# Performance work log

Hardware: AMD Instinct MI355X
Metric: run time of the kernel (lower is better)

The kernel has to match this reference:

```python
import jax, jax.numpy as jnp
import numpy as np

Z_DIM = 3
H = 128
N_BLOCKS = 4
N = 30000
E = 180000
T = 2


def _mlp2(x, W1, b1, W2, b2):
    return jnp.maximum(x @ W1 + b1, 0.0) @ W2 + b2


def _stats(x, eps=1e-8):
    # batch mean/std as accumulated by the running-stat Normalizer (buffers -> no grad)
    m = x.mean(0)
    v = jnp.maximum((x * x).mean(0) - m * m, 0.0)
    s = jnp.maximum(jnp.sqrt(v), eps)
    return jax.lax.stop_gradient(m), jax.lax.stop_gradient(s)


def setup_inputs() -> dict:
    key = jax.random.key(0)
    ks = jax.random.split(key, 32)

    def w(k, shape, fan_in):
        return jax.random.normal(k, shape, jnp.float32) / np.sqrt(fan_in).astype(np.float32)

    inp = {}
    inp["z"] = jax.random.normal(ks[0], (T, N, Z_DIM), jnp.float32)
    inp["z_target"] = jax.random.normal(ks[1], (N, Z_DIM), jnp.float32)
    inp["pos"] = jax.random.uniform(ks[2], (N, 2), jnp.float32)
    # encoder node MLP: z_dim -> H -> H
    inp["enc_node_W1"] = w(ks[3], (Z_DIM, H), Z_DIM)
    inp["enc_node_b1"] = jnp.zeros((H,), jnp.float32)
    inp["enc_node_W2"] = w(ks[4], (H, H), H)
    inp["enc_node_b2"] = jnp.zeros((H,), jnp.float32)
    # encoder edge MLP: edge_dim(3) -> H -> H
    inp["enc_edge_W1"] = w(ks[5], (3, H), 3)
    inp["enc_edge_b1"] = jnp.zeros((H,), jnp.float32)
    inp["enc_edge_W2"] = w(ks[6], (H, H), H)
    inp["enc_edge_b2"] = jnp.zeros((H,), jnp.float32)
    # decoder MLP: H -> H -> z_dim
    inp["dec_W1"] = w(ks[7], (H, H), H)
    inp["dec_b1"] = jnp.zeros((H,), jnp.float32)
    inp["dec_W2"] = w(ks[8], (H, Z_DIM), H)
    inp["dec_b2"] = jnp.zeros((Z_DIM,), jnp.float32)
    # GraphNetBlocks, stacked over n_blocks
    inp["blk_edge_W1"] = w(ks[9], (N_BLOCKS, 3 * H, H), 3 * H)
    inp["blk_edge_b1"] = jnp.zeros((N_BLOCKS, H), jnp.float32)
    inp["blk_edge_W2"] = w(ks[10], (N_BLOCKS, H, H), H)
    inp["blk_edge_b2"] = jnp.zeros((N_BLOCKS, H), jnp.float32)
    inp["blk_node_W1"] = w(ks[11], (N_BLOCKS, 2 * H, H), 2 * H)
    inp["blk_node_b1"] = jnp.zeros((N_BLOCKS, H), jnp.float32)
    inp["blk_node_W2"] = w(ks[12], (N_BLOCKS, H, H), H)
    inp["blk_node_b2"] = jnp.zeros((N_BLOCKS, H), jnp.float32)
    # bidirectional mesh edges (triangles_to_edges output)
    inp["senders"] = jax.random.randint(ks[13], (E,), 0, N, jnp.int64)
    inp["receivers"] = jax.random.randint(ks[14], (E,), 0, N, jnp.int64)
    return inp


def reference(z, z_target, pos,
              enc_node_W1, enc_node_b1, enc_node_W2, enc_node_b2,
              enc_edge_W1, enc_edge_b1, enc_edge_W2, enc_edge_b2,
              dec_W1, dec_b1, dec_W2, dec_b2,
              blk_edge_W1, blk_edge_b1, blk_edge_W2, blk_edge_b2,
              blk_node_W1, blk_node_b1, blk_node_W2, blk_node_b2,
              senders, receivers):
    zl = z[-1]                                   # [N, z_dim]
    n_nodes = zl.shape[0]

    # --- build_graph ---
    rel = pos[senders] - pos[receivers]          # [E, 2]
    ef_raw = jnp.concatenate([rel, jnp.linalg.norm(rel, axis=1, keepdims=True)], axis=1)  # [E, 3]
    em, es = _stats(ef_raw)
    ef = _mlp2((ef_raw - em) / es, enc_edge_W1, enc_edge_b1, enc_edge_W2, enc_edge_b2)    # [E, H]
    nm, ns = _stats(zl)
    nf = _mlp2((zl - nm) / ns, enc_node_W1, enc_node_b1, enc_node_W2, enc_node_b2)        # [N, H]

    # --- message passing blocks ---
    def block(carry, p):
        nf, ef = carry
        eW1, eb1, eW2, eb2, nW1, nb1, nW2, nb2 = p
        e_in = jnp.concatenate([ef, nf[senders], nf[receivers]], axis=1)   # [E, 3H]
        ef = _mlp2(e_in, eW1, eb1, eW2, eb2) + ef
        agg = jax.ops.segment_sum(ef, receivers, num_segments=n_nodes)    # [N, H]
        n_in = jnp.concatenate([nf, agg], axis=1)                          # [N, 2H]
        nf = _mlp2(n_in, nW1, nb1, nW2, nb2) + nf
        return (nf, ef), None

    (nf, ef), _ = jax.lax.scan(block, (nf, ef),
                               (blk_edge_W1, blk_edge_b1, blk_edge_W2, blk_edge_b2,
                                blk_node_W1, blk_node_b1, blk_node_W2, blk_node_b2))

    # --- decode + loss ---
    output = _mlp2(nf, dec_W1, dec_b1, dec_W2, dec_b2)                     # [N, z_dim]
    target = z_target - zl
    om, os = _stats(target)
    target_normalized = (target - om) / os
    loss = jnp.mean((target_normalized - output) ** 2)

    z_update = jax.lax.stop_gradient(output) * os + om                     # Normalizer.inverse(detach)
    z_pred = zl + z_update
    rmse = jnp.mean(jnp.sqrt(jnp.mean((z_pred - z_target) ** 2, axis=0)))
    return z_pred, loss, rmse
```

## Files before the change

### kernel.cpp

```cpp
#include <hip/hip_runtime.h>
#include <hip/hip_bf16.h>
#include <math.h>

#define HDIM 128
#define TPB 256

typedef __attribute__((ext_vector_type(8))) short bf16x8;
typedef __attribute__((ext_vector_type(4))) float f32x4;

static inline int ceil_div(int a, int b){ return (a + b - 1) / b; }

__device__ __forceinline__ float wave_sum(float v){
#pragma unroll
  for (int o = 32; o > 0; o >>= 1) v += __shfl_down(v, o, 64);
  return v;
}
__device__ __forceinline__ int wave_sum_i(int v){
#pragma unroll
  for (int o = 32; o > 0; o >>= 1) v += __shfl_down(v, o, 64);
  return v;
}

__device__ __forceinline__ short f2bf(float f){
  __hip_bfloat16 h = __float2bfloat16(f);
  return *reinterpret_cast<short*>(&h);
}
__device__ __forceinline__ float bfb2f(short s){
  unsigned int u = ((unsigned int)(unsigned short)s) << 16;
  return __builtin_bit_cast(float, u);
}

__device__ __forceinline__ void gl_lds16(const short* g, short* l){
  __builtin_amdgcn_global_load_lds(
      (const __attribute__((address_space(1))) void*)g,
      (__attribute__((address_space(3))) void*)l, 16, 0, 0);
}

__global__ void prep_a(const int* __restrict__ rcv, int* __restrict__ deg, int E, int neb,
                       const float* __restrict__ zl, const float* __restrict__ zt,
                       float* __restrict__ npart, int N, int nnb,
                       const float* __restrict__ encEW2,
                       const float* __restrict__ encNW2,
                       const float* __restrict__ decW1,
                       const float* __restrict__ beW1,
                       const float* __restrict__ beW2,
                       const float* __restrict__ bnW1,
                       const float* __restrict__ bnW2,
                       __hip_bfloat16* __restrict__ wp){
  __shared__ float red[4][12];
  const int bx = blockIdx.x, tid = threadIdx.x;
  if (bx < neb){
    int e = bx * 256 + tid;
    if (e < E) atomicAdd(&deg[rcv[e]], 1);
    return;
  }
  if (bx < neb + nnb){
    int b = bx - neb;
    int w = tid >> 6, l = tid & 63;
    int n = b * 256 + tid;
    float s[12];
#pragma unroll
    for (int i = 0; i < 12; i++) s[i] = 0.f;
    if (n < N){
#pragma unroll
      for (int d = 0; d < 3; d++){
        float z = zl[3*n+d];
        float t = zt[3*n+d] - z;
        s[d]   = z;  s[3+d] = z*z;
        s[6+d] = t;  s[9+d] = t*t;
      }
    }
#pragma unroll
    for (int i = 0; i < 12; i++) s[i] = wave_sum(s[i]);
    if (l == 0)
#pragma unroll
      for (int i = 0; i < 12; i++) red[w][i] = s[i];
    __syncthreads();
    if (tid < 12)
      npart[(size_t)b * 12 + tid] =
        red[0][tid] + red[1][tid] + red[2][tid] + red[3][tid];
    return;
  }
  int pid = bx - neb - nnb;
  int y = pid / 192;
  int x = pid - y * 192;
  const float* src; __hip_bfloat16* dst; int K;
  if (y == 0){ src = encEW2; dst = wp;          K = 128; }
  else if (y == 1){ src = encNW2; dst = wp + 16384; K = 128; }
  else if (y == 2){ src = decW1;  dst = wp + 32768; K = 128; }
  else {
    int b = (y - 3) >> 2, j = (y - 3) & 3;
    __hip_bfloat16* base = wp + 49152 + b * 114688;
    if (j == 0){ src = beW1 + b*49152; dst = base;          K = 384; }
    else if (j == 1){ src = beW2 + b*16384; dst = base + 49152; K = 128; }
    else if (j == 2){ src = bnW1 + b*32768; dst = base + 65536; K = 256; }
    else { src = bnW2 + b*16384; dst = base + 98304; K = 128; }
  }
  int id = x * 256 + tid;
  if (id >= 128 * K) return;
  int c = id >> 12;
  int r = id & 4095;
  int t = r >> 9;
  int l = (r >> 3) & 63;
  int j = r & 7;
  int k = c * 32 + ((l >> 4) << 3) + j;
  int n = t * 16 + (l & 15);
  dst[id] = __float2bfloat16(src[k * 128 + n]);
}

__global__ void scan_pass1(const int* __restrict__ deg, int* __restrict__ bsum, int N){
  __shared__ int red[4];
  int tid = threadIdx.x;
  int base = blockIdx.x * 1024;
  int s = 0;
  for (int i = tid; i < 1024; i += 256){
    int idx = base + i;
    if (idx < N) s += deg[idx];
  }
  s = wave_sum_i(s);
  if ((tid & 63) == 0) red[tid >> 6] = s;
  __syncthreads();
  if (tid == 0) bsum[blockIdx.x] = red[0] + red[1] + red[2] + red[3];
}

__global__ void scan_pass3(const int* __restrict__ deg, const int* __restrict__ bsum,
                           int nsb, int* __restrict__ cursor, int N){
  __shared__ int tsum[256];
  __shared__ int base_s;
  int tid = threadIdx.x;
  if (tid == 0){
    int acc = 0;
    for (int b = 0; b < (int)blockIdx.x; b++) acc += bsum[b];
    base_s = acc;
  }
  int base = blockIdx.x * 1024;
  int i0 = base + tid * 4;
  int v[4];
  int s = 0;
#pragma unroll
  for (int k = 0; k < 4; k++){
    int idx = i0 + k;
    v[k] = (idx < N) ? deg[idx] : 0;
    s += v[k];
  }
  tsum[tid] = s;
  __syncthreads();
  for (int off = 1; off < 256; off <<= 1){
    int val = (tid >= off) ? tsum[tid - off] : 0;
    __syncthreads();
    tsum[tid] += val;
    __syncthreads();
  }
  int excl = (tid == 0) ? 0 : tsum[tid - 1];
  int b = base_s + excl;
#pragma unroll
  for (int k = 0; k < 4; k++){
    int idx = i0 + k;
    if (idx < N){
      cursor[idx] = b;
      b += v[k];
    }
  }
}

__global__ void edge_prep(const float* __restrict__ pos,
                          const int* __restrict__ snd,
                          const int* __restrict__ rcv,
                          int* __restrict__ cursor,
                          int* __restrict__ psnd,
                          int* __restrict__ prcv,
                          float* __restrict__ ef_raw,
                          float* __restrict__ epart,
                          const float* __restrict__ npart, int nn,
                          float* __restrict__ fin,
                          unsigned int* __restrict__ ep_cnt,
                          int E, int N){
  __shared__ float red[4][6];
  __shared__ float rawS[18];
  __shared__ float redS[4];
  __shared__ int doneS;
  int tid = threadIdx.x, w = tid >> 6, l = tid & 63;
  int e = blockIdx.x * blockDim.x + tid;
  float s[6] = {0.f,0.f,0.f,0.f,0.f,0.f};
  if (e < E){
    int si = snd[e], ri = rcv[e];
    int p = atomicAdd(&cursor[ri], 1);
    psnd[p] = si;
    prcv[p] = ri;
    float rx = pos[2*si]   - pos[2*ri];
    float ry = pos[2*si+1] - pos[2*ri+1];
    float nm = sqrtf(rx*rx + ry*ry);
    ef_raw[3*p]   = rx;
    ef_raw[3*p+1] = ry;
    ef_raw[3*p+2] = nm;
    s[0] = rx; s[1] = ry; s[2] = nm;
    s[3] = rx*rx; s[4] = ry*ry; s[5] = nm*nm;
  }
#pragma unroll
  for (int k = 0; k < 6; k++) s[k] = wave_sum(s[k]);
  if (l == 0)
#pragma unroll
    for (int k = 0; k < 6; k++) red[w][k] = s[k];
  __syncthreads();
  if (tid < 6)
    epart[(size_t)blockIdx.x * 6 + tid] =
      red[0][tid] + red[1][tid] + red[2][tid] + red[3][tid];
  __syncthreads();
  if (tid == 0){
    __threadfence();
    unsigned int t = atomicAdd(ep_cnt, 1u);
    doneS = (t == gridDim.x - 1);
  }
  __syncthreads();
  if (!doneS) return;
  const int ne = gridDim.x;
  for (int j = 0; j < 6; j++){
    float t = 0.f;
    for (int b = tid; b < ne; b += 256) t += epart[(size_t)b * 6 + j];
    t = wave_sum(t);
    if (l == 0) redS[w] = t;
    __syncthreads();
    if (tid == 0) rawS[j] = redS[0] + redS[1] + redS[2] + redS[3];
    __syncthreads();
  }
  for (int j = 0; j < 12; j++){
    float t = 0.f;
    for (int b = tid; b < nn; b += 256) t += npart[(size_t)b * 12 + j];
    t = wave_sum(t);
    if (l == 0) redS[w] = t;
    __syncthreads();
    if (tid == 0) rawS[6 + j] = redS[0] + redS[1] + redS[2] + redS[3];
    __syncthreads();
  }
  if (tid == 0){
#pragma unroll
    for (int d = 0; d < 3; d++){
      float cE = (float)E, cN = (float)N;
      float m, v;
      m = rawS[0+d] / cE; v = fmaxf(rawS[3+d]/cE - m*m, 0.f);
      fin[0+d] = m;  fin[3+d]  = fmaxf(sqrtf(v), 1e-8f);
      m = rawS[6+d] / cN; v = fmaxf(rawS[9+d]/cN - m*m, 0.f);
      fin[6+d] = m;  fin[9+d]  = fmaxf(sqrtf(v), 1e-8f);
      m = rawS[12+d] / cN; v = fmaxf(rawS[15+d]/cN - m*m, 0.f);
      fin[12+d] = m; fin[15+d] = fmaxf(sqrtf(v), 1e-8f);
    }
  }
}

__launch_bounds__(256)
__global__ void encoder_both(const float* __restrict__ eraw,
                             const float* __restrict__ zl,
                             const float* __restrict__ fin,
                             const float* __restrict__ eW1, const float* __restrict__ eb1,
                             const float* __restrict__ nW1, const float* __restrict__ nb1,
                             const __hip_bfloat16* __restrict__ wp,
                             const float* __restrict__ eb2, const float* __restrict__ nb2,
                             __hip_bfloat16* __restrict__ efo, __hip_bfloat16* __restrict__ nfo,
                             int E, int N, int EB){
  __shared__ __align__(16) short bsh[16384];
  const int tid = threadIdx.x, w = tid >> 6, l = tid & 63, m = l & 15, q = l >> 4;
  const bool ise = ((int)blockIdx.x < EB);
  const float* raw = ise ? eraw : zl;
  const float* mptr = fin + (ise ? 0 : 6);
  const float* sptr = fin + (ise ? 3 : 9);
  const float* W1 = ise ? eW1 : nW1;
  const float* b1 = ise ? eb1 : nb1;
  const float* b2 = ise ? eb2 : nb2;
  const short* wsrc = (const short*)wp + (ise ? 0 : 16384);
  __hip_bfloat16* out = ise ? efo : nfo;
  const int rows = ise ? E : N;
  const int bx = ise ? (int)blockIdx.x : (int)blockIdx.x - EB;
#pragma unroll
  for (int i = 0; i < 8; i++){
    int inst = w * 8 + i;
    gl_lds16(wsrc + inst * 512 + l * 8, &bsh[inst * 512]);
  }
  float s0 = mptr[0], s1 = mptr[1], s2 = mptr[2];
  float d0 = sptr[0], d1 = sptr[1], d2 = sptr[2];
  const int row0 = bx * 64 + w * 16;
  const int ra = min(row0 + m, rows - 1);
  float x0 = (raw[3*ra]   - s0) / d0;
  float x1 = (raw[3*ra+1] - s1) / d1;
  float x2 = (raw[3*ra+2] - s2) / d2;
  bf16x8 afr[4];
#pragma unroll
  for (int c = 0; c < 4; c++){
    int nb = c * 32 + q * 8;
#pragma unroll
    for (int j = 0; j < 8; j++){
      float h = b1[nb+j] + x0 * W1[nb+j] + x1 * W1[128+nb+j] + x2 * W1[256+nb+j];
      afr[c][j] = f2bf(fmaxf(h, 0.f));
    }
  }
  f32x4 acc[8];
#pragma unroll
  for (int t = 0; t < 8; t++) acc[t] = (f32x4){0.f,0.f,0.f,0.f};
  __syncthreads();
#pragma unroll
  for (int c = 0; c < 4; c++){
#pragma unroll
    for (int t = 0; t < 8; t++){
      bf16x8 b = *(const bf16x8*)&bsh[(c*8 + t)*512 + l*8];
      acc[t] = __builtin_amdgcn_mfma_f32_16x16x32_bf16(afr[c], b, acc[t], 0, 0, 0);
    }
  }
  const int row_d = row0 + q * 4;
#pragma unroll
  for (int t = 0; t < 8; t++){
    int col = t * 16 + m;
    float bb = b2[col];
#pragma unroll
    for (int r = 0; r < 4; r++){
      int e = row_d + r;
      if (e < rows) out[(size_t)e * HDIM + col] = __float2bfloat16(acc[t][r] + bb);
    }
  }
}

__launch_bounds__(256)
__global__ void msg_pre(const __hip_bfloat16* __restrict__ nf,
                        const __hip_bfloat16* __restrict__ eWf,
                        __hip_bfloat16* __restrict__ u,
                        float* __restrict__ agg, int N){
  __shared__ __align__(16) short wsh[16384];
  const int tid = threadIdx.x, w = tid >> 6, l = tid & 63, m = l & 15, q = l >> 4;
  const short* wsrc = (const short*)eWf + 4 * 4096;
#pragma unroll
  for (int i = 0; i < 8; i++){
    int f = w * 8 + i;
    gl_lds16(wsrc + f * 512 + l * 8, &wsh[f * 512]);
  }
  {
    float* az = agg + (size_t)blockIdx.x * 8192;
#pragma unroll
    for (int i = 0; i < 8; i++)
      *(f32x4*)(az + (size_t)(i * 256 + tid) * 4) = (f32x4){0.f,0.f,0.f,0.f};
  }
  const int row0 = blockIdx.x * 64 + w * 16;
  const int ra = min(row0 + m, N - 1);
  const short* pa = (const short*)nf + (size_t)ra * HDIM + q * 8;
  bf16x8 afr[4];
#pragma unroll
  for (int c = 0; c < 4; c++) afr[c] = *(const bf16x8*)(pa + c * 32);
  f32x4 acc[8];
#pragma unroll
  for (int t = 0; t < 8; t++) acc[t] = (f32x4){0.f,0.f,0.f,0.f};
  __syncthreads();
#pragma unroll
  for (int c = 0; c < 4; c++)
#pragma unroll
    for (int t = 0; t < 8; t++){
      bf16x8 b = *(const bf16x8*)&wsh[(c*8 + t)*512 + l*8];
      acc[t] = __builtin_amdgcn_mfma_f32_16x16x32_bf16(afr[c], b, acc[t], 0, 0, 0);
    }
  const int row_d = row0 + q * 4;
#pragma unroll
  for (int t = 0; t < 8; t++){
    int col = t * 16 + m;
#pragma unroll
    for (int r = 0; r < 4; r++){
      int n = row_d + r;
      if (n < N) u[(size_t)n * 256 + col] = __float2bfloat16(acc[t][r]);
    }
  }
  __syncthreads();
#pragma unroll
  for (int i = 0; i < 8; i++){
    int f = w * 8 + i;
    gl_lds16(wsrc + 16384 + f * 512 + l * 8, &wsh[f * 512]);
  }
#pragma unroll
  for (int t = 0; t < 8; t++) acc[t] = (f32x4){0.f,0.f,0.f,0.f};
  __syncthreads();
#pragma unroll
  for (int c = 0; c < 4; c++)
#pragma unroll
    for (int t = 0; t < 8; t++){
      bf16x8 b = *(const bf16x8*)&wsh[(c*8 + t)*512 + l*8];
      acc[t] = __builtin_amdgcn_mfma_f32_16x16x32_bf16(afr[c], b, acc[t], 0, 0, 0);
    }
#pragma unroll
  for (int t = 0; t < 8; t++){
    int col = 128 + t * 16 + m;
#pragma unroll
    for (int r = 0; r < 4; r++){
      int n = row_d + r;
      if (n < N) u[(size_t)n * 256 + col] = __float2bfloat16(acc[t][r]);
    }
  }
}

__launch_bounds__(512)
__global__ void edge_block(const int* __restrict__ psnd,
                           const int* __restrict__ prcv,
                           const __hip_bfloat16* __restrict__ u,
                           __hip_bfloat16* __restrict__ ef,
                           const __hip_bfloat16* __restrict__ Wfrag,
                           const float* __restrict__ b1,
                           const float* __restrict__ b2,
                           float* __restrict__ agg,
                           int do_write, int E){
  __shared__ __align__(16) short bsh[16384];
  __shared__ __align__(16) short hsh[8][16][136];
  __shared__ int rsh[128];
  const int tid = threadIdx.x, w = tid >> 6, l = tid & 63, m = l & 15, q = l >> 4;
  const short* wsrc = (const short*)Wfrag;
  const int row0 = blockIdx.x * 128 + w * 16;
  const int grow = min(row0 + (l >> 2), E - 1);
  const int us_row = psnd[grow], ur_row = prcv[grow];
  if ((l & 3) == 0) rsh[w * 16 + (l >> 2)] = ur_row;
#pragma unroll
  for (int i = 0; i < 4; i++){
    int inst = i * 8 + w;
    gl_lds16(wsrc + inst * 512 + l * 8, &bsh[inst * 512]);
  }
  const int ra = min(row0 + m, E - 1);
  const short* pe = (const short*)ef + (size_t)ra * HDIM + q * 8;
  bf16x8 afr[4];
#pragma unroll
  for (int c = 0; c < 4; c++) afr[c] = *(const bf16x8*)(pe + c * 32);
  {
    const short* pus = (const short*)u + (size_t)us_row * 256 + (l & 3) * 32;
    const short* pur = (const short*)u + (size_t)ur_row * 256 + 128 + (l & 3) * 32;
    short* hdst = &hsh[w][l >> 2][(l & 3) * 32];
#pragma unroll
    for (int k = 0; k < 4; k++){
      bf16x8 a = *(const bf16x8*)(pus + k * 8);
      bf16x8 b = *(const bf16x8*)(pur + k * 8);
      bf16x8 s;
#pragma unroll
      for (int j = 0; j < 8; j++) s[j] = f2bf(bfb2f(a[j]) + bfb2f(b[j]));
      *(bf16x8*)(hdst + k * 8) = s;
    }
  }
  f32x4 acc[8];
#pragma unroll
  for (int t = 0; t < 8; t++) acc[t] = (f32x4){0.f,0.f,0.f,0.f};
  __syncthreads();
#pragma unroll
  for (int c = 0; c < 4; c++){
#pragma unroll
    for (int t = 0; t < 8; t++){
      bf16x8 b = *(const bf16x8*)&bsh[(c*8 + t)*512 + l*8];
      acc[t] = __builtin_amdgcn_mfma_f32_16x16x32_bf16(afr[c], b, acc[t], 0, 0, 0);
    }
  }
  __syncthreads();
#pragma unroll
  for (int i = 0; i < 4; i++){
    int inst = i * 8 + w;
    gl_lds16(wsrc + 49152 + inst * 512 + l * 8, &bsh[inst * 512]);
  }
#pragma unroll
  for (int t = 0; t < 8; t++){
    float bb = b1[t * 16 + m];
#pragma unroll
    for (int r = 0; r < 4; r++){
      float uval = bfb2f(hsh[w][q*4 + r][t*16 + m]);
      hsh[w][q*4 + r][t*16 + m] = f2bf(fmaxf(acc[t][r] + uval + bb, 0.f));
    }
  }
  __syncthreads();
  bf16x8 ah[4];
  const short* ph = &hsh[w][m][0] + q * 8;
#pragma unroll
  for (int c = 0; c < 4; c++) ah[c] = *(const bf16x8*)(ph + c * 32);
#pragma unroll
  for (int t = 0; t < 8; t++) acc[t] = (f32x4){0.f,0.f,0.f,0.f};
#pragma unroll
  for (int c = 0; c < 4; c++){
#pragma unroll
    for (int t = 0; t < 8; t++){
      bf16x8 b = *(const bf16x8*)&bsh[(c*8 + t)*512 + l*8];
      acc[t] = __builtin_amdgcn_mfma_f32_16x16x32_bf16(ah[c], b, acc[t], 0, 0, 0);
    }
  }
#pragma unroll
  for (int t = 0; t < 8; t++){
    float bb = b2[t * 16 + m];
#pragma unroll
    for (int r = 0; r < 4; r++)
      hsh[w][q*4 + r][t*16 + m] = f2bf(acc[t][r] + bb);
  }
  const int orow = row0 + (l >> 2);
  const int orc = min(orow, E - 1);
  const short* pold = (const short*)ef + (size_t)orc * HDIM + (l & 3) * 32;
  short* hslot = &hsh[w][l >> 2][(l & 3) * 32];
  short* dst = (short*)ef + (size_t)orc * HDIM + (l & 3) * 32;
  const bool wr = (orow < E) && do_write;
#pragma unroll
  for (int k = 0; k < 4; k++){
    bf16x8 vnew = *(const bf16x8*)(hslot + k * 8);
    bf16x8 vo   = *(const bf16x8*)(pold + k * 8);
    bf16x8 vr;
#pragma unroll
    for (int j = 0; j < 8; j++) vr[j] = f2bf(bfb2f(vnew[j]) + bfb2f(vo[j]));
    *(bf16x8*)(hslot + k * 8) = vr;
    if (wr) *(bf16x8*)(dst + k * 8) = vr;
  }
  __syncthreads();
  {
    const int c = tid & 127;
    const int g = tid >> 7;
    const int nval = min(128, E - (int)blockIdx.x * 128);
    const int e0 = g * 32;
    if (e0 < nval){
      const int e1 = min(e0 + 32, nval);
      float run = 0.f; int cur = -1; int runstart = e0;
#pragma unroll
      for (int half = 0; half < 2; half++){
        float v[16]; int rv[16];
#pragma unroll
        for (int k = 0; k < 16; k++){
          int e = e0 + half * 16 + k;
          v[k]  = bfb2f(hsh[(e >> 4) & 7][e & 15][c]);
          rv[k] = rsh[e & 127];
        }
#pragma unroll
        for (int k = 0; k < 16; k++){
          int e = e0 + half * 16 + k;
          if (e < e1){
            if (rv[k] != cur){
              if (cur >= 0){
                if (runstart == e0) atomicAdd(&agg[(size_t)cur * 128 + c], run);
                else                agg[(size_t)cur * 128 + c] = run;
              }
              cur = rv[k]; run = 0.f; runstart = e;
            }
            run += v[k];
          }
        }
      }
      atomicAdd(&agg[(size_t)cur * 128 + c], run);
    }
  }
}

#define NB_COMPUTE_CHUNK(c) do {                                               \
  const short* bb_ = &bsh[(((c) >> 1) & 1) * 8192 + ((c) & 1) * 4096];         \
  _Pragma("unroll")                                                            \
  for (int t = 0; t < 8; t++){                                                 \
    bf16x8 b = *(const bf16x8*)(bb_ + t * 512 + l * 8);                        \
    acc[t] = __builtin_amdgcn_mfma_f32_16x16x32_bf16(afr[c], b, acc[t], 0, 0, 0); \
  }                                                                            \
} while(0)

__launch_bounds__(256)
__global__ void node_block(const float* __restrict__ agg,
                           __hip_bfloat16* __restrict__ nf,
                           const __hip_bfloat16* __restrict__ Wfrag,
                           const float* __restrict__ b1,
                           const float* __restrict__ b2,
                           const __hip_bfloat16* __restrict__ eWf_next,
                           __hip_bfloat16* __restrict__ u,
                           float* __restrict__ aggz,
                           int mode,
                           const __hip_bfloat16* __restrict__ decWf,
                           const float* __restrict__ db1,
                           const float* __restrict__ dW2,
                           const float* __restrict__ db2,
                           const float* __restrict__ zl,
                           const float* __restrict__ z_target,
                           const float* __restrict__ fin,
                           float* __restrict__ d_out,
                           float* __restrict__ lred,
                           unsigned int* __restrict__ cnt,
                           int N){
  __shared__ __align__(16) short bsh[16384];
  __shared__ __align__(16) short hsh[4][16][136];
  __shared__ float Wl[HDIM * 3];
  __shared__ float redS[4][4];
  const int tid = threadIdx.x, w = tid >> 6, l = tid & 63, m = l & 15, q = l >> 4;
  const short* wsrc = (const short*)Wfrag;
  auto stage_pair = [&](int p){
    const short* s = wsrc + p * 8192;
    short* d = &bsh[(p & 1) * 8192];
#pragma unroll
    for (int i = 0; i < 4; i++)
      gl_lds16(s + (i*4 + w)*512 + l*8, d + (i*4 + w)*512);
  };
  stage_pair(0); stage_pair(1);

  const int row0 = blockIdx.x * 64 + w * 16;
  const int ra = min(row0 + m, N - 1);
  const short* pn = (const short*)nf + (size_t)ra * HDIM + q * 8;
  bf16x8 afr[8];
#pragma unroll
  for (int c = 0; c < 4; c++) afr[c] = *(const bf16x8*)(pn + c * 32);

  const float* pag = agg + (size_t)ra * 128 + q * 8;
#pragma unroll
  for (int c = 0; c < 4; c++){
    f32x4 a0 = *(const f32x4*)(pag + c * 32);
    f32x4 a1 = *(const f32x4*)(pag + c * 32 + 4);
#pragma unroll
    for (int j = 0; j < 4; j++){
      afr[4 + c][j]     = f2bf(a0[j]);
      afr[4 + c][4 + j] = f2bf(a1[j]);
    }
  }

  f32x4 acc[8];
#pragma unroll
  for (int t = 0; t < 8; t++) acc[t] = (f32x4){0.f,0.f,0.f,0.f};
  __syncthreads();
  if (mode == 0){
    float* az = aggz + (size_t)blockIdx.x * 8192;
#pragma unroll
    for (int i = 0; i < 8; i++)
      *(f32x4*)(az + (size_t)(i * 256 + tid) * 4) = (f32x4){0.f,0.f,0.f,0.f};
  }
  NB_COMPUTE_CHUNK(0);
  NB_COMPUTE_CHUNK(1);
  __syncthreads();
  stage_pair(2);
  NB_COMPUTE_CHUNK(2);
  NB_COMPUTE_CHUNK(3);
  __syncthreads();
  stage_pair(3);
  NB_COMPUTE_CHUNK(4);
  NB_COMPUTE_CHUNK(5);
  __syncthreads();
  NB_COMPUTE_CHUNK(6);
  NB_COMPUTE_CHUNK(7);
  __syncthreads();
  {
    const short* s = wsrc + 32768;
#pragma unroll
    for (int i = 0; i < 8; i++)
      gl_lds16(s + (i*4 + w)*512 + l*8, &bsh[(i*4 + w)*512]);
  }
#pragma unroll
  for (int t = 0; t < 8; t++){
    float bb = b1[t * 16 + m];
#pragma unroll
    for (int r = 0; r < 4; r++)
      hsh[w][q*4 + r][t*16 + m] = f2bf(fmaxf(acc[t][r] + bb, 0.f));
  }
  __syncthreads();
  const short* ph = &hsh[w][m][0] + q * 8;
#pragma unroll
  for (int t = 0; t < 8; t++) acc[t] = (f32x4){0.f,0.f,0.f,0.f};
#pragma unroll
  for (int c = 0; c < 4; c++){
    bf16x8 a = *(const bf16x8*)(ph + c * 32);
#pragma unroll
    for (int t = 0; t < 8; t++){
      bf16x8 b = *(const bf16x8*)&bsh[(c*8 + t)*512 + l*8];
      acc[t] = __builtin_amdgcn_mfma_f32_16x16x32_bf16(a, b, acc[t], 0, 0, 0);
    }
  }
#pragma unroll
  for (int t = 0; t < 8; t++){
    float bb = b2[t * 16 + m];
#pragma unroll
    for (int r = 0; r < 4; r++)
      hsh[w][q*4 + r][t*16 + m] = f2bf(acc[t][r] + bb);
  }
  {
    const int orow = row0 + (l >> 2);
    const int orc = min(orow, N - 1);
    const short* pold = (const short*)nf + (size_t)orc * HDIM + (l & 3) * 32;
    short* hslot = &hsh[w][l >> 2][(l & 3) * 32];
    short* dst = (short*)nf + (size_t)orc * HDIM + (l & 3) * 32;
    const bool wr = (orow < N) && (mode == 0);
#pragma unroll
    for (int k = 0; k < 4; k++){
      bf16x8 vnew = *(const bf16x8*)(hslot + k * 8);
      bf16x8 vo   = *(const bf16x8*)(pold + k * 8);
      bf16x8 vr;
#pragma unroll
      for (int j = 0; j < 8; j++) vr[j] = f2bf(bfb2f(vnew[j]) + bfb2f(vo[j]));
      *(bf16x8*)(hslot + k * 8) = vr;
      if (wr) *(bf16x8*)(dst + k * 8) = vr;
    }
  }

  if (mode == 0){
    const short* ws = (const short*)eWf_next + 4 * 4096;
#pragma unroll
    for (int i = 0; i < 8; i++){
      int f = w * 8 + i;
      gl_lds16(ws + f * 512 + l * 8, &bsh[f * 512]);
    }
    __syncthreads();
    bf16x8 a2[4];
    const short* ph2 = &hsh[w][m][0] + q * 8;
#pragma unroll
    for (int c = 0; c < 4; c++) a2[c] = *(const bf16x8*)(ph2 + c * 32);
#pragma unroll
    for (int t = 0; t < 8; t++) acc[t] = (f32x4){0.f,0.f,0.f,0.f};
#pragma unroll
    for (int c = 0; c < 4; c++)
#pragma unroll
      for (int t = 0; t < 8; t++){
        bf16x8 b = *(const bf16x8*)&bsh[(c*8 + t)*512 + l*8];
        acc[t] = __builtin_amdgcn_mfma_f32_16x16x32_bf16(a2[c], b, acc[t], 0, 0, 0);
      }
    const int row_d = row0 + q * 4;
#pragma unroll
    for (int t = 0; t < 8; t++){
      int col = t * 16 + m;
#pragma unroll
      for (int r = 0; r < 4; r++){
        int n = row_d + r;
        if (n < N) u[(size_t)n * 256 + col] = __float2bfloat16(acc[t][r]);
      }
    }
    __syncthreads();
#pragma unroll
    for (int i = 0; i < 8; i++){
      int f = w * 8 + i;
      gl_lds16(ws + 16384 + f * 512 + l * 8, &bsh[f * 512]);
    }
#pragma unroll
    for (int t = 0; t < 8; t++) acc[t] = (f32x4){0.f,0.f,0.f,0.f};
    __syncthreads();
#pragma unroll
    for (int c = 0; c < 4; c++)
#pragma unroll
      for (int t = 0; t < 8; t++){
        bf16x8 b = *(const bf16x8*)&bsh[(c*8 + t)*512 + l*8];
        acc[t] = __builtin_amdgcn_mfma_f32_16x16x32_bf16(a2[c], b, acc[t], 0, 0, 0);
      }
#pragma unroll
    for (int t = 0; t < 8; t++){
      int col = 128 + t * 16 + m;
#pragma unroll
      for (int r = 0; r < 4; r++){
        int n = row_d + r;
        if (n < N) u[(size_t)n * 256 + col] = __float2bfloat16(acc[t][r]);
      }
    }
  } else {
    const short* ws = (const short*)decWf;
#pragma unroll
    for (int i = 0; i < 8; i++){
      int f = w * 8 + i;
      gl_lds16(ws + f * 512 + l * 8, &bsh[f * 512]);
    }
    for (int i = tid; i < HDIM * 3; i += 256) Wl[i] = dW2[i];
    __syncthreads();
    bf16x8 a2[4];
    const short* ph2 = &hsh[w][m][0] + q * 8;
#pragma unroll
    for (int c = 0; c < 4; c++) a2[c] = *(const bf16x8*)(ph2 + c * 32);
#pragma unroll
    for (int t = 0; t < 8; t++) acc[t] = (f32x4){0.f,0.f,0.f,0.f};
#pragma unroll
    for (int c = 0; c < 4; c++)
#pragma unroll
      for (int t = 0; t < 8; t++){
        bf16x8 b = *(const bf16x8*)&bsh[(c*8 + t)*512 + l*8];
        acc[t] = __builtin_amdgcn_mfma_f32_16x16x32_bf16(a2[c], b, acc[t], 0, 0, 0);
      }
    float p0[4] = {0,0,0,0}, p1[4] = {0,0,0,0}, p2[4] = {0,0,0,0};
#pragma unroll
    for (int t = 0; t < 8; t++){
      int col = t * 16 + m;
      float bb = db1[col];
      float w0 = Wl[col*3], w1 = Wl[col*3+1], w2 = Wl[col*3+2];
#pragma unroll
      for (int r = 0; r < 4; r++){
        float h = fmaxf(acc[t][r] + bb, 0.f);
        p0[r] += h * w0; p1[r] += h * w1; p2[r] += h * w2;
      }
    }
#pragma unroll
    for (int r = 0; r < 4; r++){
#pragma unroll
      for (int o = 1; o < 16; o <<= 1){
        p0[r] += __shfl_xor(p0[r], o, 64);
        p1[r] += __shfl_xor(p1[r], o, 64);
        p2[r] += __shfl_xor(p2[r], o, 64);
      }
    }
    float s[4] = {0.f,0.f,0.f,0.f};
    if (m == 0){
#pragma unroll
      for (int r = 0; r < 4; r++){
        int n = row0 + q * 4 + r;
        if (n < N){
          float pd[3] = {p0[r], p1[r], p2[r]};
#pragma unroll
          for (int d = 0; d < 3; d++){
            float o   = pd[d] + db2[d];
            float om = fin[12 + d], os = fin[15 + d];
            float zld = zl[3*n + d];
            float zt  = z_target[3*n + d];
            float tn  = ((zt - zld) - om) / os;
            float diff = tn - o;
            s[0] += diff * diff;
            float zp = zld + o * os + om;
            d_out[3*n + d] = zp;
            float e = zp - zt;
            s[1 + d] += e * e;
          }
        }
      }
    }
#pragma unroll
    for (int k = 0; k < 4; k++) s[k] = wave_sum(s[k]);
    if (l == 0)
#pragma unroll
      for (int k = 0; k < 4; k++) redS[w][k] = s[k];
    __syncthreads();
    if (tid < 4)
      atomicAdd(&lred[tid], redS[0][tid] + redS[1][tid] + redS[2][tid] + redS[3][tid]);
    __syncthreads();
    if (tid == 0){
      __threadfence();
      unsigned int t = atomicAdd(cnt, 1u);
      if (t == gridDim.x - 1){
        float vals[4];
#pragma unroll
        for (int k = 0; k < 4; k++) vals[k] = atomicAdd(&lred[k], 0.f);
        float cN = (float)N;
        float loss = vals[0] / (3.f * cN);
        float rmse = (sqrtf(vals[1]/cN) + sqrtf(vals[2]/cN) + sqrtf(vals[3]/cN)) / 3.f;
        d_out[(size_t)3 * N]     = loss;
        d_out[(size_t)3 * N + 1] = rmse;
      }
    }
  }
}

extern "C" void kernel_launch(void* const* d_in, const int* in_sizes, int n_in,
                              void* d_out, int out_size, void* d_ws, size_t ws_size,
                              hipStream_t stream){
  const float* z           = (const float*)d_in[0];
  const float* z_target    = (const float*)d_in[1];
  const float* pos         = (const float*)d_in[2];
  const float* enc_node_W1 = (const float*)d_in[3];
  const float* enc_node_b1 = (const float*)d_in[4];
  const float* enc_node_W2 = (const float*)d_in[5];
  const float* enc_node_b2 = (const float*)d_in[6];
  const float* enc_edge_W1 = (const float*)d_in[7];
  const float* enc_edge_b1 = (const float*)d_in[8];
  const float* enc_edge_W2 = (const float*)d_in[9];
  const float* enc_edge_b2 = (const float*)d_in[10];
  const float* dec_W1      = (const float*)d_in[11];
  const float* dec_b1      = (const float*)d_in[12];
  const float* dec_W2      = (const float*)d_in[13];
  const float* dec_b2      = (const float*)d_in[14];
  const float* blk_edge_W1 = (const float*)d_in[15];
  const float* blk_edge_b1 = (const float*)d_in[16];
  const float* blk_edge_W2 = (const float*)d_in[17];
  const float* blk_edge_b2 = (const float*)d_in[18];
  const float* blk_node_W1 = (const float*)d_in[19];
  const float* blk_node_b1 = (const float*)d_in[20];
  const float* blk_node_W2 = (const float*)d_in[21];
  const float* blk_node_b2 = (const float*)d_in[22];
  const int*   senders     = (const int*)d_in[23];
  const int*   receivers   = (const int*)d_in[24];

  const int N = in_sizes[1] / 3;
  const int E = in_sizes[23];
  const float* zl = z + (size_t)N * 3;

  const int neb = ceil_div(E, TPB);
  const int nnb = ceil_div(N, TPB);
  const int nsb = ceil_div(N, 1024);
  const int EB  = ceil_div(E, 64);
  const int NB  = ceil_div(N, 64);

  char* p = (char*)d_ws;
  auto carve = [&](size_t bytes) -> char* {
    char* r = p; p += (bytes + 255) & ~(size_t)255; return r;
  };
  float* stats_fin = (float*)carve(32 * 4);
  float* epart     = (float*)carve((size_t)neb * 6 * 4);
  float* npart     = (float*)carve((size_t)nnb * 12 * 4);
  float* ef_raw    = (float*)carve((size_t)E * 3 * 4);
  int*   deg       = (int*)carve((size_t)(N + 16) * 4);
  float* lred      = (float*)(deg + N);
  unsigned int* cnt    = (unsigned int*)(deg + N + 4);
  unsigned int* ep_cnt = (unsigned int*)(deg + N + 5);
  int*   bsum      = (int*)carve((size_t)(nsb + 1) * 4);
  int*   cursor    = (int*)carve((size_t)N * 4);
  int*   psnd      = (int*)carve((size_t)E * 4);
  int*   prcv      = (int*)carve((size_t)E * 4);
  float* agg       = (float*)carve(((size_t)N + 64) * 128 * 4);
  __hip_bfloat16* wp = (__hip_bfloat16*)carve((size_t)507904 * 2);
  __hip_bfloat16* ef = (__hip_bfloat16*)carve((size_t)E * HDIM * 2);
  __hip_bfloat16* nf = (__hip_bfloat16*)carve((size_t)N * HDIM * 2);
  __hip_bfloat16* u  = (__hip_bfloat16*)carve((size_t)N * 256 * 2);

  float* out = (float*)d_out;

  hipMemsetAsync(deg, 0, (size_t)(N + 16) * 4, stream);

  prep_a<<<neb + nnb + 3648, TPB, 0, stream>>>(receivers, deg, E, neb,
                                               zl, z_target, npart, N, nnb,
                                               enc_edge_W2, enc_node_W2, dec_W1,
                                               blk_edge_W1, blk_edge_W2,
                                               blk_node_W1, blk_node_W2, wp);
  scan_pass1<<<nsb, TPB, 0, stream>>>(deg, bsum, N);
  scan_pass3<<<nsb, TPB, 0, stream>>>(deg, bsum, nsb, cursor, N);
  edge_prep<<<neb, TPB, 0, stream>>>(pos, senders, receivers, cursor,
                                     psnd, prcv, ef_raw, epart,
                                     npart, nnb, stats_fin, ep_cnt, E, N);

  encoder_both<<<EB + NB, TPB, 0, stream>>>(ef_raw, zl, stats_fin,
                                            enc_edge_W1, enc_edge_b1,
                                            enc_node_W1, enc_node_b1,
                                            wp, enc_edge_b2, enc_node_b2,
                                            ef, nf, E, N, EB);

  msg_pre<<<NB, TPB, 0, stream>>>(nf, wp + 49152, u, agg, N);

  for (int b = 0; b < 4; b++){
    const __hip_bfloat16* eWf = wp + 49152 + (size_t)b * 114688;
    const __hip_bfloat16* nWf = eWf + 65536;
    const float* eb1 = blk_edge_b1 + (size_t)b * 128;
    const float* eb2 = blk_edge_b2 + (size_t)b * 128;
    const float* nb1 = blk_node_b1 + (size_t)b * 128;
    const float* nb2 = blk_node_b2 + (size_t)b * 128;
    const __hip_bfloat16* eWf_next =
        wp + 49152 + (size_t)((b + 1) & 3) * 114688;

    edge_block<<<ceil_div(E, 128), 512, 0, stream>>>(psnd, prcv, u, ef,
                                                     eWf, eb1, eb2, agg,
                                                     (b < 3) ? 1 : 0, E);
    node_block<<<NB, TPB, 0, stream>>>(agg, nf, nWf, nb1, nb2,
                                       eWf_next, u, agg,
                                       (b < 3) ? 0 : 1,
                                       wp + 32768, dec_b1, dec_W2, dec_b2,
                                       zl, z_target, stats_fin,
                                       out, lred, cnt, N);
  }
}
```

Baseline: 500.9 us.

## Unfuse next-block message precompute from node kernel into per-block msg_pre launch

```diff
diff --git a/kernel.cpp b/kernel.cpp
--- a/kernel.cpp
+++ b/kernel.cpp
@@ -213,6 +213,7 @@
   }
   __syncthreads();
   if (!doneS) return;
+  __threadfence();
   const int ne = gridDim.x;
   for (int j = 0; j < 6; j++){
     float t = 0.f;
@@ -551,9 +552,6 @@
                            const __hip_bfloat16* __restrict__ Wfrag,
                            const float* __restrict__ b1,
                            const float* __restrict__ b2,
-                           const __hip_bfloat16* __restrict__ eWf_next,
-                           __hip_bfloat16* __restrict__ u,
-                           float* __restrict__ aggz,
                            int mode,
                            const __hip_bfloat16* __restrict__ decWf,
                            const float* __restrict__ db1,
@@ -604,12 +602,6 @@
 #pragma unroll
   for (int t = 0; t < 8; t++) acc[t] = (f32x4){0.f,0.f,0.f,0.f};
   __syncthreads();
-  if (mode == 0){
-    float* az = aggz + (size_t)blockIdx.x * 8192;
-#pragma unroll
-    for (int i = 0; i < 8; i++)
-      *(f32x4*)(az + (size_t)(i * 256 + tid) * 4) = (f32x4){0.f,0.f,0.f,0.f};
-  }
   NB_COMPUTE_CHUNK(0);
   NB_COMPUTE_CHUNK(1);
   __syncthreads();
@@ -675,152 +667,96 @@
       if (wr) *(bf16x8*)(dst + k * 8) = vr;
     }
   }
-
-  if (mode == 0){
-    const short* ws = (const short*)eWf_next + 4 * 4096;
-#pragma unroll
-    for (int i = 0; i < 8; i++){
-      int f = w * 8 + i;
-      gl_lds16(ws + f * 512 + l * 8, &bsh[f * 512]);
-    }
-    __syncthreads();
-    bf16x8 a2[4];
-    const short* ph2 = &hsh[w][m][0] + q * 8;
-#pragma unroll
-    for (int c = 0; c < 4; c++) a2[c] = *(const bf16x8*)(ph2 + c * 32);
-#pragma unroll
-    for (int t = 0; t < 8; t++) acc[t] = (f32x4){0.f,0.f,0.f,0.f};
-#pragma unroll
-    for (int c = 0; c < 4; c++)
-#pragma unroll
-      for (int t = 0; t < 8; t++){
-        bf16x8 b = *(const bf16x8*)&bsh[(c*8 + t)*512 + l*8];
-        acc[t] = __builtin_amdgcn_mfma_f32_16x16x32_bf16(a2[c], b, acc[t], 0, 0, 0);
-      }
-    const int row_d = row0 + q * 4;
+  if (mode == 0) return;
+
+  __syncthreads();
+  {
+    const short* ws = (const short*)decWf;
+#pragma unroll
+    for (int i = 0; i < 8; i++)
+      gl_lds16(ws + (i*4 + w)*512 + l*8, &bsh[(i*4 + w)*512]);
+  }
+  for (int i = tid; i < HDIM * 3; i += 256) Wl[i] = dW2[i];
+  __syncthreads();
+  bf16x8 a2[4];
+  const short* ph2 = &hsh[w][m][0] + q * 8;
+#pragma unroll
+  for (int c = 0; c < 4; c++) a2[c] = *(const bf16x8*)(ph2 + c * 32);
+#pragma unroll
+  for (int t = 0; t < 8; t++) acc[t] = (f32x4){0.f,0.f,0.f,0.f};
+#pragma unroll
+  for (int c = 0; c < 4; c++)
 #pragma unroll
     for (int t = 0; t < 8; t++){
-      int col = t * 16 + m;
-#pragma unroll
-      for (int r = 0; r < 4; r++){
-        int n = row_d + r;
-        if (n < N) u[(size_t)n * 256 + col] = __float2bfloat16(acc[t][r]);
-      }
-    }
-    __syncthreads();
-#pragma unroll
-    for (int i = 0; i < 8; i++){
-      int f = w * 8 + i;
-      gl_lds16(ws + 16384 + f * 512 + l * 8, &bsh[f * 512]);
-    }
-#pragma unroll
-    for (int t = 0; t < 8; t++) acc[t] = (f32x4){0.f,0.f,0.f,0.f};
-    __syncthreads();
-#pragma unroll
-    for (int c = 0; c < 4; c++)
-#pragma unroll
-      for (int t = 0; t < 8; t++){
-        bf16x8 b = *(const bf16x8*)&bsh[(c*8 + t)*512 + l*8];
-        acc[t] = __builtin_amdgcn_mfma_f32_16x16x32_bf16(a2[c], b, acc[t], 0, 0, 0);
-      }
-#pragma unroll
-    for (int t = 0; t < 8; t++){
-      int col = 128 + t * 16 + m;
-#pragma unroll
-      for (int r = 0; r < 4; r++){
-        int n = row_d + r;
-        if (n < N) u[(size_t)n * 256 + col] = __float2bfloat16(acc[t][r]);
-      }
-    }
-  } else {
-    const short* ws = (const short*)decWf;
-#pragma unroll
-    for (int i = 0; i < 8; i++){
-      int f = w * 8 + i;
-      gl_lds16(ws + f * 512 + l * 8, &bsh[f * 512]);
-    }
-    for (int i = tid; i < HDIM * 3; i += 256) Wl[i] = dW2[i];
-    __syncthreads();
-    bf16x8 a2[4];
-    const short* ph2 = &hsh[w][m][0] + q * 8;
-#pragma unroll
-    for (int c = 0; c < 4; c++) a2[c] = *(const bf16x8*)(ph2 + c * 32);
-#pragma unroll
-    for (int t = 0; t < 8; t++) acc[t] = (f32x4){0.f,0.f,0.f,0.f};
-#pragma unroll
-    for (int c = 0; c < 4; c++)
-#pragma unroll
-      for (int t = 0; t < 8; t++){
-        bf16x8 b = *(const bf16x8*)&bsh[(c*8 + t)*512 + l*8];
-        acc[t] = __builtin_amdgcn_mfma_f32_16x16x32_bf16(a2[c], b, acc[t], 0, 0, 0);
-      }
-    float p0[4] = {0,0,0,0}, p1[4] = {0,0,0,0}, p2[4] = {0,0,0,0};
-#pragma unroll
-    for (int t = 0; t < 8; t++){
-      int col = t * 16 + m;
-      float bb = db1[col];
-      float w0 = Wl[col*3], w1 = Wl[col*3+1], w2 = Wl[col*3+2];
-#pragma unroll
-      for (int r = 0; r < 4; r++){
-        float h = fmaxf(acc[t][r] + bb, 0.f);
-        p0[r] += h * w0; p1[r] += h * w1; p2[r] += h * w2;
-      }
-    }
+      bf16x8 b = *(const bf16x8*)&bsh[(c*8 + t)*512 + l*8];
+      acc[t] = __builtin_amdgcn_mfma_f32_16x16x32_bf16(a2[c], b, acc[t], 0, 0, 0);
+    }
+  float p0[4] = {0,0,0,0}, p1[4] = {0,0,0,0}, p2[4] = {0,0,0,0};
+#pragma unroll
+  for (int t = 0; t < 8; t++){
+    int col = t * 16 + m;
+    float bb = db1[col];
+    float w0 = Wl[col*3], w1 = Wl[col*3+1], w2 = Wl[col*3+2];
 #pragma unroll
     for (int r = 0; r < 4; r++){
-#pragma unroll
-      for (int o = 1; o < 16; o <<= 1){
-        p0[r] += __shfl_xor(p0[r], o, 64);
-        p1[r] += __shfl_xor(p1[r], o, 64);
-        p2[r] += __shfl_xor(p2[r], o, 64);
-      }
-    }
-    float s[4] = {0.f,0.f,0.f,0.f};
-    if (m == 0){
-#pragma unroll
-      for (int r = 0; r < 4; r++){
-        int n = row0 + q * 4 + r;
-        if (n < N){
-          float pd[3] = {p0[r], p1[r], p2[r]};
-#pragma unroll
-          for (int d = 0; d < 3; d++){
-            float o   = pd[d] + db2[d];
-            float om = fin[12 + d], os = fin[15 + d];
-            float zld = zl[3*n + d];
-            float zt  = z_target[3*n + d];
-            float tn  = ((zt - zld) - om) / os;
-            float diff = tn - o;
-            s[0] += diff * diff;
-            float zp = zld + o * os + om;
-            d_out[3*n + d] = zp;
-            float e = zp - zt;
-            s[1 + d] += e * e;
-          }
+      float h = fmaxf(acc[t][r] + bb, 0.f);
+      p0[r] += h * w0; p1[r] += h * w1; p2[r] += h * w2;
+    }
+  }
+#pragma unroll
+  for (int r = 0; r < 4; r++){
+#pragma unroll
+    for (int o = 1; o < 16; o <<= 1){
+      p0[r] += __shfl_xor(p0[r], o, 64);
+      p1[r] += __shfl_xor(p1[r], o, 64);
+      p2[r] += __shfl_xor(p2[r], o, 64);
+    }
+  }
+  float s[4] = {0.f,0.f,0.f,0.f};
+  if (m == 0){
+#pragma unroll
+    for (int r = 0; r < 4; r++){
+      int n = row0 + q * 4 + r;
+      if (n < N){
+        float pd[3] = {p0[r], p1[r], p2[r]};
+#pragma unroll
+        for (int d = 0; d < 3; d++){
+          float o   = pd[d] + db2[d];
+          float om = fin[12 + d], os = fin[15 + d];
+          float zld = zl[3*n + d];
+          float zt  = z_target[3*n + d];
+          float tn  = ((zt - zld) - om) / os;
+          float diff = tn - o;
+          s[0] += diff * diff;
+          float zp = zld + o * os + om;
+          d_out[3*n + d] = zp;
+          float e = zp - zt;
+          s[1 + d] += e * e;
         }
       }
     }
-#pragma unroll
-    for (int k = 0; k < 4; k++) s[k] = wave_sum(s[k]);
-    if (l == 0)
-#pragma unroll
-      for (int k = 0; k < 4; k++) redS[w][k] = s[k];
-    __syncthreads();
-    if (tid < 4)
-      atomicAdd(&lred[tid], redS[0][tid] + redS[1][tid] + redS[2][tid] + redS[3][tid]);
-    __syncthreads();
-    if (tid == 0){
-      __threadfence();
-      unsigned int t = atomicAdd(cnt, 1u);
-      if (t == gridDim.x - 1){
-        float vals[4];
-#pragma unroll
-        for (int k = 0; k < 4; k++) vals[k] = atomicAdd(&lred[k], 0.f);
-        float cN = (float)N;
-        float loss = vals[0] / (3.f * cN);
-        float rmse = (sqrtf(vals[1]/cN) + sqrtf(vals[2]/cN) + sqrtf(vals[3]/cN)) / 3.f;
-        d_out[(size_t)3 * N]     = loss;
-        d_out[(size_t)3 * N + 1] = rmse;
-      }
+  }
+#pragma unroll
+  for (int k = 0; k < 4; k++) s[k] = wave_sum(s[k]);
+  if (l == 0)
+#pragma unroll
+    for (int k = 0; k < 4; k++) redS[w][k] = s[k];
+  __syncthreads();
+  if (tid < 4)
+    atomicAdd(&lred[tid], redS[0][tid] + redS[1][tid] + redS[2][tid] + redS[3][tid]);
+  __syncthreads();
+  if (tid == 0){
+    __threadfence();
+    unsigned int t = atomicAdd(cnt, 1u);
+    if (t == gridDim.x - 1){
+      float vals[4];
+#pragma unroll
+      for (int k = 0; k < 4; k++) vals[k] = atomicAdd(&lred[k], 0.f);
+      float cN = (float)N;
+      float loss = vals[0] / (3.f * cN);
+      float rmse = (sqrtf(vals[1]/cN) + sqrtf(vals[2]/cN) + sqrtf(vals[3]/cN)) / 3.f;
+      d_out[(size_t)3 * N]     = loss;
+      d_out[(size_t)3 * N + 1] = rmse;
     }
   }
 }
@@ -907,8 +843,6 @@
                                             wp, enc_edge_b2, enc_node_b2,
                                             ef, nf, E, N, EB);
 
-  msg_pre<<<NB, TPB, 0, stream>>>(nf, wp + 49152, u, agg, N);
-
   for (int b = 0; b < 4; b++){
     const __hip_bfloat16* eWf = wp + 49152 + (size_t)b * 114688;
     const __hip_bfloat16* nWf = eWf + 65536;
@@ -916,14 +850,12 @@
     const float* eb2 = blk_edge_b2 + (size_t)b * 128;
     const float* nb1 = blk_node_b1 + (size_t)b * 128;
     const float* nb2 = blk_node_b2 + (size_t)b * 128;
-    const __hip_bfloat16* eWf_next =
-        wp + 49152 + (size_t)((b + 1) & 3) * 114688;
-
+
+    msg_pre<<<NB, TPB, 0, stream>>>(nf, eWf, u, agg, N);
     edge_block<<<ceil_div(E, 128), 512, 0, stream>>>(psnd, prcv, u, ef,
                                                      eWf, eb1, eb2, agg,
                                                      (b < 3) ? 1 : 0, E);
     node_block<<<NB, TPB, 0, stream>>>(agg, nf, nWf, nb1, nb2,
-                                       eWf_next, u, agg,
                                        (b < 3) ? 0 : 1,
                                        wp + 32768, dec_b1, dec_W2, dec_b2,
                                        zl, z_target, stats_fin,
```

After: 511.3 us. 1.02x slower.
